# Optimization experiments

Hardware: AMD Instinct MI355X
Metric: run time of the kernel (lower is better)

Reference implementation:

```python
import jax, jax.numpy as jnp
import numpy as np

D_MODEL = 1024
NUM_HEADS = 16
HEAD_DIM = D_MODEL // NUM_HEADS


def setup_inputs() -> dict:
    key = jax.random.key(0)
    ks = jax.random.split(key, 10)
    B, SQ, SKV = 2, 2048, 2048
    s = 1.0 / np.sqrt(D_MODEL)
    inp = {
        "query": jax.random.normal(ks[0], (B, SQ, D_MODEL), jnp.float32),
        "key_value": jax.random.normal(ks[1], (B, SKV, D_MODEL), jnp.float32),
        "Wq": jax.random.normal(ks[2], (D_MODEL, D_MODEL), jnp.float32) * s,
        "bq": jnp.zeros((D_MODEL,), jnp.float32),
        "Wk": jax.random.normal(ks[3], (D_MODEL, D_MODEL), jnp.float32) * s,
        "bk": jnp.zeros((D_MODEL,), jnp.float32),
        "Wv": jax.random.normal(ks[4], (D_MODEL, D_MODEL), jnp.float32) * s,
        "bv": jnp.zeros((D_MODEL,), jnp.float32),
        "Wo": jax.random.normal(ks[5], (D_MODEL, D_MODEL), jnp.float32) * s,
        "bo": jnp.zeros((D_MODEL,), jnp.float32),
    }
    return inp


def reference(query, key_value, Wq, bq, Wk, bk, Wv, bv, Wo, bo):
    B, SQ, _ = query.shape
    SKV = key_value.shape[1]
    # projections (torch Linear: x @ W^T + b)
    Q = query @ Wq.T + bq
    K = key_value @ Wk.T + bk
    V = key_value @ Wv.T + bv
    # [B, H, S, Dh]
    Q = Q.reshape(B, SQ, NUM_HEADS, HEAD_DIM).transpose(0, 2, 1, 3)
    K = K.reshape(B, SKV, NUM_HEADS, HEAD_DIM).transpose(0, 2, 1, 3)
    V = V.reshape(B, SKV, NUM_HEADS, HEAD_DIM).transpose(0, 2, 1, 3)
    scores = jnp.einsum("bhqd,bhkd->bhqk", Q, K) / np.sqrt(HEAD_DIM)
    # causal mask: position q may attend to kv positions <= q
    causal = jnp.tril(jnp.ones((SQ, SKV), bool))  # True = keep
    scores = jnp.where(causal[None, None], scores, -jnp.inf)
    attn = jax.nn.softmax(scores, axis=-1)
    # dropout is identity in eval mode
    out = jnp.einsum("bhqk,bhkd->bhqd", attn, V)
    out = out.transpose(0, 2, 1, 3).reshape(B, SQ, D_MODEL)
    return out @ Wo.T + bo
```

## Files before the change

### kernel.cpp

```cpp
#include <hip/hip_runtime.h>
#include <hip/hip_bf16.h>
#include <cstdint>
#include <type_traits>

#define DM 1024
#define HEADS 16
#define DH 64
#define SEQ 2048
#define BATCH 2

typedef __attribute__((ext_vector_type(8))) short bf16x8;
typedef __attribute__((ext_vector_type(4))) float f32x4;
typedef __attribute__((ext_vector_type(16))) float f32x16;
typedef __attribute__((ext_vector_type(2))) unsigned int u32x2;
typedef __attribute__((ext_vector_type(4))) unsigned int u32x4;

#define SCALE2 0.18033688011112042f

#define GLOAD(dst, ptr) \
    asm volatile("global_load_dwordx4 %0, %1, off" : "=v"(dst) : "v"(ptr) : "memory")

static __device__ __forceinline__ unsigned short f2bf(float f) {
    unsigned u = __builtin_bit_cast(unsigned, f);
    u = u + 0x7fffu + ((u >> 16) & 1u);
    return (unsigned short)(u >> 16);
}

__global__ __launch_bounds__(256) void cast_all_k(
    const float* __restrict__ q, const float* __restrict__ kv,
    const float* __restrict__ wq, const float* __restrict__ wk,
    const float* __restrict__ wv, const float* __restrict__ wo,
    unsigned short* __restrict__ qb, unsigned short* __restrict__ kvb,
    unsigned short* __restrict__ wqb, unsigned short* __restrict__ wkb,
    unsigned short* __restrict__ wvb, unsigned short* __restrict__ wob)
{
    int blk = blockIdx.x;
    const float* s; unsigned short* d; int base;
    if (blk < 2048)      { s = q;  d = qb;  base = 0; }
    else if (blk < 4096) { s = kv; d = kvb; base = 2048; }
    else if (blk < 4608) { s = wq; d = wqb; base = 4096; }
    else if (blk < 5120) { s = wk; d = wkb; base = 4608; }
    else if (blk < 5632) { s = wv; d = wvb; base = 5120; }
    else                 { s = wo; d = wob; base = 5632; }
    int i = ((blk - base) * 256 + threadIdx.x) * 8;
    float4 a = *(const float4*)(s + i);
    float4 b2 = *(const float4*)(s + i + 4);
    ushort4 o0, o1;
    o0.x = f2bf(a.x);  o0.y = f2bf(a.y);  o0.z = f2bf(a.z);  o0.w = f2bf(a.w);
    o1.x = f2bf(b2.x); o1.y = f2bf(b2.y); o1.z = f2bf(b2.z); o1.w = f2bf(b2.w);
    *(ushort4*)(d + i) = o0;
    *(ushort4*)(d + i + 4) = o1;
}

template<int EPI>
__global__ __launch_bounds__(256) void gemm_nt(
    const unsigned short* __restrict__ A,
    const unsigned short* __restrict__ Bw,
    const float* __restrict__ biasA,
    const float* __restrict__ biasB,
    void* __restrict__ out0,
    void* __restrict__ out1,
    int M, int N, int K)
{
    constexpr int BK = 64;
    __shared__ alignas(16) unsigned short As[64 * BK];
    __shared__ alignas(16) unsigned short Bs[128 * BK];

    const int t = threadIdx.x;
    const int lane = t & 63;
    const int w = t >> 6;
    const int wn = w * 32;
    const int lr = lane & 15, lg = lane >> 4;
    const int m0 = blockIdx.x * 64, n0 = blockIdx.y * 128;

    f32x4 acc[4][2] = {};

    const int srow = t >> 3;
    const int schunk = t & 7;

    for (int kt = 0; kt < K; kt += BK) {
#pragma unroll
        for (int c = 0; c < 2; c++) {
            int row = srow + c * 32;
            int gc = schunk ^ (row & 7);
            __builtin_amdgcn_global_load_lds(
                (const __attribute__((address_space(1))) unsigned int*)(A + (size_t)(m0 + row) * K + kt + gc * 8),
                (__attribute__((address_space(3))) unsigned int*)(&As[row * BK + schunk * 8]), 16, 0, 0);
        }
#pragma unroll
        for (int c = 0; c < 4; c++) {
            int row = srow + c * 32;
            int gc = schunk ^ (row & 7);
            __builtin_amdgcn_global_load_lds(
                (const __attribute__((address_space(1))) unsigned int*)(Bw + (size_t)(n0 + row) * K + kt + gc * 8),
                (__attribute__((address_space(3))) unsigned int*)(&Bs[row * BK + schunk * 8]), 16, 0, 0);
        }
        __syncthreads();
#pragma unroll
        for (int kk = 0; kk < 2; kk++) {
            bf16x8 af[4], bfr[2];
#pragma unroll
            for (int i = 0; i < 4; i++)
                af[i] = *(const bf16x8*)(&As[(i * 16 + lr) * BK + (((kk * 4 + lg) ^ (lr & 7))) * 8]);
#pragma unroll
            for (int jj = 0; jj < 2; jj++)
                bfr[jj] = *(const bf16x8*)(&Bs[(wn + jj * 16 + lr) * BK + (((kk * 4 + lg) ^ (lr & 7))) * 8]);
#pragma unroll
            for (int i = 0; i < 4; i++)
#pragma unroll
                for (int jj = 0; jj < 2; jj++)
                    acc[i][jj] = __builtin_amdgcn_mfma_f32_16x16x32_bf16(af[i], bfr[jj], acc[i][jj], 0, 0, 0);
        }
        __syncthreads();
    }

    if constexpr (EPI == 0) {
        unsigned short* C = (unsigned short*)out0;
#pragma unroll
        for (int i = 0; i < 4; i++) {
            int rbase = m0 + i * 16 + lg * 4;
#pragma unroll
            for (int jj = 0; jj < 2; jj++) {
                int col = n0 + wn + jj * 16 + lr;
                float bv = biasA[col];
#pragma unroll
                for (int r = 0; r < 4; r++)
                    C[(size_t)(rbase + r) * 1024 + col] = f2bf((acc[i][jj][r] + bv) * SCALE2);
            }
        }
    } else if constexpr (EPI == 1) {
        if (n0 < 1024) {
            unsigned short* C = (unsigned short*)out0;
#pragma unroll
            for (int i = 0; i < 4; i++) {
                int rbase = m0 + i * 16 + lg * 4;
#pragma unroll
                for (int jj = 0; jj < 2; jj++) {
                    int col = n0 + wn + jj * 16 + lr;
                    float bv = biasA[col];
#pragma unroll
                    for (int r = 0; r < 4; r++)
                        C[(size_t)(rbase + r) * 1024 + col] = f2bf(acc[i][jj][r] + bv);
                }
            }
        } else {
            unsigned short* C = (unsigned short*)out1;
            int bidx = m0 >> 11;
#pragma unroll
            for (int i = 0; i < 4; i++) {
                int s0 = (m0 & 2047) + i * 16 + lg * 4;
#pragma unroll
                for (int jj = 0; jj < 2; jj++) {
                    int nv = n0 - 1024 + wn + jj * 16 + lr;
                    float bv = biasB[nv];
                    int hh = nv >> 6, dd = nv & 63;
                    ushort4 st;
                    st.x = f2bf(acc[i][jj][0] + bv);
                    st.y = f2bf(acc[i][jj][1] + bv);
                    st.z = f2bf(acc[i][jj][2] + bv);
                    st.w = f2bf(acc[i][jj][3] + bv);
                    *(ushort4*)(C + ((size_t)((bidx * HEADS + hh) * DH + dd)) * SEQ + s0) = st;
                }
            }
        }
    } else {
        float* C = (float*)out0;
#pragma unroll
        for (int i = 0; i < 4; i++) {
            int rbase = m0 + i * 16 + lg * 4;
#pragma unroll
            for (int jj = 0; jj < 2; jj++) {
                int col = n0 + wn + jj * 16 + lr;
                float bv = biasA[col];
#pragma unroll
                for (int r = 0; r < 4; r++)
                    C[(size_t)(rbase + r) * 1024 + col] = acc[i][jj][r] + bv;
            }
        }
    }
}

__global__ __launch_bounds__(256, 2) void attn_k(
    const unsigned short* __restrict__ Qp,
    const unsigned short* __restrict__ Kp,
    const unsigned short* __restrict__ Vt,
    unsigned short* __restrict__ Ctx)
{
    __shared__ alignas(16) unsigned char ldsb[2 * 16384];

    const int lane = threadIdx.x & 63;
    const int w = threadIdx.x >> 6;
    const int x = blockIdx.x;
    const int bh = x & 31;
    const int i16 = x >> 5;
    const int c = (i16 < 8) ? (2 * i16) : (31 - 2 * i16);
    const int b = bh >> 4, h = bh & 15;
    const int q0 = c * 128;
    const int lq = lane & 31;
    const int hi = lane >> 5;
    const int qq = q0 + w * 32 + lq;
    const int nb = 2 * c + 2;
    const int my_nb = (q0 + 32 * w + 95) >> 6;
    constexpr float THR = 11.5f;

    bf16x8 Qf[4];
    {
        u32x4 qtmp[4];
        const unsigned short* qb = Qp + (size_t)(b * SEQ + qq) * DM + h * DH + hi * 8;
#pragma unroll
        for (int d = 0; d < 4; d++) GLOAD(qtmp[d], qb + d * 16);
        asm volatile("s_waitcnt vmcnt(0)" ::: "memory");
        __builtin_amdgcn_sched_barrier(0);
#pragma unroll
        for (int d = 0; d < 4; d++) Qf[d] = __builtin_bit_cast(bf16x8, qtmp[d]);
    }

    const int colx = (((lane & 7) ^ (lane >> 3)) << 4);
    const char* kg[2];
    const char* vg[2];
#pragma unroll
    for (int u = 0; u < 2; u++) {
        int s = 2 * w + u;
        int row = 8 * s + (lane >> 3);
        kg[u] = (const char*)Kp + (((size_t)(b * SEQ + row) * DM + h * DH) * 2) + colx;
        vg[u] = (const char*)Vt + ((((size_t)(b * HEADS + h) * DH + row) * SEQ) * 2) + colx;
    }
    const int kxor = (lq & 7) << 4;

    auto stage = [&](int buf, int t) {
        int kboff_k = t * (64 * DM * 2);
        int kboff_v = t * 128;
#pragma unroll
        for (int u = 0; u < 2; u++) {
            int s = 2 * w + u;
            __builtin_amdgcn_global_load_lds(
                (const __attribute__((address_space(1))) unsigned int*)(kg[u] + kboff_k),
                (__attribute__((address_space(3))) unsigned int*)(&ldsb[buf * 16384 + s * 1024 + lane * 16]), 16, 0, 0);
            __builtin_amdgcn_global_load_lds(
                (const __attribute__((address_space(1))) unsigned int*)(vg[u] + kboff_v),
                (__attribute__((address_space(3))) unsigned int*)(&ldsb[buf * 16384 + 8192 + s * 1024 + lane * 16]), 16, 0, 0);
        }
    };

    f32x16 o0 = {}, o1 = {};
    float m_run = -1e30f, l_run = 0.f;
    const int qmh0 = qq - 4 * hi;

    stage(0, 0);

    for (int t = 0; t < nb; t++) {
        const int cur = t & 1;
        if (t + 1 < nb) {
            stage(cur ^ 1, t + 1);
            asm volatile("s_waitcnt vmcnt(4)" ::: "memory");
        } else {
            asm volatile("s_waitcnt vmcnt(0)" ::: "memory");
        }
        __builtin_amdgcn_sched_barrier(0);
        __builtin_amdgcn_s_barrier();

        if (t < my_nb) {
            const unsigned char* Kb = &ldsb[cur * 16384];
            const unsigned char* Vb = Kb + 8192;
            const int kb = t * 64;

            bf16x8 KA[4], KB[4], Vc[4][2];
#pragma unroll
            for (int d = 0; d < 4; d++) {
                int col = (d * 32 + hi * 16) ^ kxor;
                KA[d] = *(const bf16x8*)(Kb + lq * 128 + col);
                KB[d] = *(const bf16x8*)(Kb + (lq + 32) * 128 + col);
            }
#pragma unroll
            for (int s = 0; s < 4; s++)
#pragma unroll
                for (int dt = 0; dt < 2; dt++)
                    Vc[s][dt] = *(const bf16x8*)(Vb + (dt * 32 + lq) * 128 + ((s * 32 + hi * 16) ^ kxor));

            f32x16 sa0 = {}, sa1 = {};
            __builtin_amdgcn_s_setprio(1);
#pragma unroll
            for (int d = 0; d < 4; d++) {
                sa0 = __builtin_amdgcn_mfma_f32_32x32x16_bf16(KA[d], Qf[d], sa0, 0, 0, 0);
                sa1 = __builtin_amdgcn_mfma_f32_32x32x16_bf16(KB[d], Qf[d], sa1, 0, 0, 0);
            }
            __builtin_amdgcn_s_setprio(0);

            const int qmh = qmh0 - kb;
#pragma unroll
            for (int r = 0; r < 16; r++) {
                int kvl = (r & 3) + 8 * (r >> 2);
                sa0[r] = (kvl <= qmh) ? sa0[r] : -1e30f;
                sa1[r] = (kvl + 32 <= qmh) ? sa1[r] : -1e30f;
            }
            float mx[16];
#pragma unroll
            for (int r = 0; r < 16; r++) mx[r] = fmaxf(sa0[r], sa1[r]);
#pragma unroll
            for (int r = 0; r < 8; r++) mx[r] = fmaxf(mx[r], mx[r + 8]);
#pragma unroll
            for (int r = 0; r < 4; r++) mx[r] = fmaxf(mx[r], mx[r + 4]);
            mx[0] = fmaxf(mx[0], mx[2]);
            mx[1] = fmaxf(mx[1], mx[3]);
            float mloc = fmaxf(mx[0], mx[1]);
            mloc = fmaxf(mloc, __shfl_xor(mloc, 32));

            if (!__all(mloc - m_run <= THR)) {
                float m_new = fmaxf(m_run, mloc);
                float sf = __builtin_amdgcn_exp2f(m_run - m_new);
                l_run *= sf;
#pragma unroll
                for (int r = 0; r < 16; r++) { o0[r] *= sf; o1[r] *= sf; }
                m_run = m_new;
            }

            float p0v[16], p1v[16];
#pragma unroll
            for (int r = 0; r < 16; r++) {
                p0v[r] = __builtin_amdgcn_exp2f(sa0[r] - m_run);
                p1v[r] = __builtin_amdgcn_exp2f(sa1[r] - m_run);
            }
            float s4[8];
#pragma unroll
            for (int r = 0; r < 8; r++) s4[r] = (p0v[r] + p0v[r + 8]) + (p1v[r] + p1v[r + 8]);
#pragma unroll
            for (int r = 0; r < 4; r++) s4[r] += s4[r + 4];
            float ps = (s4[0] + s4[1]) + (s4[2] + s4[3]);
            ps += __shfl_xor(ps, 32);
            l_run += ps;

            unsigned c0[8], c1[8];
#pragma unroll
            for (int ii = 0; ii < 8; ii++) {
                unsigned pk;
                asm("v_cvt_pk_bf16_f32 %0, %1, %2" : "=v"(pk) : "v"(p0v[2 * ii]), "v"(p0v[2 * ii + 1]));
                c0[ii] = pk;
                asm("v_cvt_pk_bf16_f32 %0, %1, %2" : "=v"(pk) : "v"(p1v[2 * ii]), "v"(p1v[2 * ii + 1]));
                c1[ii] = pk;
            }
            bf16x8 Pb[4];
            {
                u32x2 r02 = __builtin_amdgcn_permlane32_swap(c0[0], c0[2], false, false);
                u32x2 r13 = __builtin_amdgcn_permlane32_swap(c0[1], c0[3], false, false);
                u32x2 r46 = __builtin_amdgcn_permlane32_swap(c0[4], c0[6], false, false);
                u32x2 r57 = __builtin_amdgcn_permlane32_swap(c0[5], c0[7], false, false);
                u32x4 w0 = {r02.x, r13.x, r02.y, r13.y};
                u32x4 w1 = {r46.x, r57.x, r46.y, r57.y};
                Pb[0] = __builtin_bit_cast(bf16x8, w0);
                Pb[1] = __builtin_bit_cast(bf16x8, w1);
            }
            {
                u32x2 r02 = __builtin_amdgcn_permlane32_swap(c1[0], c1[2], false, false);
                u32x2 r13 = __builtin_amdgcn_permlane32_swap(c1[1], c1[3], false, false);
                u32x2 r46 = __builtin_amdgcn_permlane32_swap(c1[4], c1[6], false, false);
                u32x2 r57 = __builtin_amdgcn_permlane32_swap(c1[5], c1[7], false, false);
                u32x4 w0 = {r02.x, r13.x, r02.y, r13.y};
                u32x4 w1 = {r46.x, r57.x, r46.y, r57.y};
                Pb[2] = __builtin_bit_cast(bf16x8, w0);
                Pb[3] = __builtin_bit_cast(bf16x8, w1);
            }

            __builtin_amdgcn_s_setprio(1);
#pragma unroll
            for (int s = 0; s < 4; s++) {
                o0 = __builtin_amdgcn_mfma_f32_32x32x16_bf16(Vc[s][0], Pb[s], o0, 0, 0, 0);
                o1 = __builtin_amdgcn_mfma_f32_32x32x16_bf16(Vc[s][1], Pb[s], o1, 0, 0, 0);
            }
            __builtin_amdgcn_s_setprio(0);
        }
        __builtin_amdgcn_s_barrier();
    }

    float inv = 1.0f / l_run;
    unsigned short* cb = Ctx + (size_t)(b * SEQ + qq) * DM + h * DH + hi * 4;
#pragma unroll
    for (int g = 0; g < 4; g++) {
        ushort4 s0, s1;
        s0.x = f2bf(o0[4 * g + 0] * inv); s0.y = f2bf(o0[4 * g + 1] * inv);
        s0.z = f2bf(o0[4 * g + 2] * inv); s0.w = f2bf(o0[4 * g + 3] * inv);
        s1.x = f2bf(o1[4 * g + 0] * inv); s1.y = f2bf(o1[4 * g + 1] * inv);
        s1.z = f2bf(o1[4 * g + 2] * inv); s1.w = f2bf(o1[4 * g + 3] * inv);
        *(ushort4*)(cb + g * 8) = s0;
        *(ushort4*)(cb + 32 + g * 8) = s1;
    }
}

extern "C" void kernel_launch(void* const* d_in, const int* in_sizes, int n_in,
                              void* d_out, int out_size, void* d_ws, size_t ws_size,
                              hipStream_t stream)
{
    const float* query = (const float*)d_in[0];
    const float* keyv  = (const float*)d_in[1];
    const float* Wq = (const float*)d_in[2];
    const float* bq = (const float*)d_in[3];
    const float* Wk = (const float*)d_in[4];
    const float* bk = (const float*)d_in[5];
    const float* Wv = (const float*)d_in[6];
    const float* bv = (const float*)d_in[7];
    const float* Wo = (const float*)d_in[8];
    const float* bo = (const float*)d_in[9];
    float* out = (float*)d_out;

    const int M = BATCH * SEQ;
    char* ws = (char*)d_ws;
    size_t off = 0;
    auto alloc = [&](size_t elems) { unsigned short* p = (unsigned short*)(ws + off); off += elems * 2; return p; };
    unsigned short* qb  = alloc((size_t)M * DM);
    unsigned short* kvb = alloc((size_t)M * DM);
    unsigned short* wqb = alloc((size_t)DM * DM);
    unsigned short* wkb = alloc((size_t)DM * DM);
    unsigned short* wvb = alloc((size_t)DM * DM);
    unsigned short* wob = alloc((size_t)DM * DM);
    unsigned short* Qp  = alloc((size_t)M * DM);
    unsigned short* Kp  = alloc((size_t)M * DM);
    unsigned short* Vt  = alloc((size_t)M * DM);
    unsigned short* Ctx = alloc((size_t)M * DM);

    cast_all_k<<<6144, 256, 0, stream>>>(query, keyv, Wq, Wk, Wv, Wo,
                                         qb, kvb, wqb, wkb, wvb, wob);

    gemm_nt<0><<<dim3(M / 64, 8),  256, 0, stream>>>(qb,  wqb, bq, nullptr, Qp, nullptr, M, DM, DM);
    gemm_nt<1><<<dim3(M / 64, 16), 256, 0, stream>>>(kvb, wkb, bk, bv,      Kp, Vt,      M, 2 * DM, DM);

    attn_k<<<dim3(512), 256, 0, stream>>>(Qp, Kp, Vt, Ctx);

    gemm_nt<2><<<dim3(M / 64, 8),  256, 0, stream>>>(Ctx, wob, bo, nullptr, out, nullptr, M, DM, DM);
}
```

Measured before the change: 119.8 us.

## Split causal attention KV range across blocks and add a combine kernel

Query chunks with longer causal KV ranges are split into 2–4 blocks, each covering a contiguous KV slice. The grid grows from 512 to 1280 blocks, which is meant to even out the per-block work imbalance that comes from the causal mask. Each split writes unnormalized bf16 partial outputs plus its running max and sum into workspace regions whose earlier contents are no longer needed. A new combine kernel merges the partials with log-sum-exp weights. The cost is an extra launch, extra global traffic for the partials, and an added bf16 rounding step on the partial outputs.

After: 122.3 us. 1.02x slower.

```diff
diff --git a/kernel.cpp b/kernel.cpp
--- a/kernel.cpp
+++ b/kernel.cpp
@@ -24,6 +24,9 @@
     unsigned u = __builtin_bit_cast(unsigned, f);
     u = u + 0x7fffu + ((u >> 16) & 1u);
     return (unsigned short)(u >> 16);
+}
+static __device__ __forceinline__ float bf2f(unsigned short us) {
+    return __builtin_bit_cast(float, (unsigned)us << 16);
 }
 
 __global__ __launch_bounds__(256) void cast_all_k(
@@ -184,7 +187,9 @@
     const unsigned short* __restrict__ Qp,
     const unsigned short* __restrict__ Kp,
     const unsigned short* __restrict__ Vt,
-    unsigned short* __restrict__ Ctx)
+    unsigned short* __restrict__ Ctx,
+    unsigned short* __restrict__ pO,
+    float2* __restrict__ pML)
 {
     __shared__ alignas(16) unsigned char ldsb[2 * 16384];
 
@@ -192,14 +197,22 @@
     const int w = threadIdx.x >> 6;
     const int x = blockIdx.x;
     const int bh = x & 31;
-    const int i16 = x >> 5;
-    const int c = (i16 < 8) ? (2 * i16) : (31 - 2 * i16);
+    const int g = x >> 5;
+    int c, p, S;
+    if (g < 4)       { c = g;                    p = 0;            S = 1; }
+    else if (g < 12) { c = 4 + ((g - 4) >> 1);   p = (g - 4) & 1;  S = 2; }
+    else if (g < 24) { c = 8 + (g - 12) / 3;     p = (g - 12) % 3; S = 3; }
+    else             { c = 12 + ((g - 24) >> 2); p = (g - 24) & 3; S = 4; }
+    const int nb = 2 * c + 2;
+    const int len0 = (nb + S - 1) / S;
+    const int start = p * len0;
+    const int len = min(len0, nb - start);
+
     const int b = bh >> 4, h = bh & 15;
     const int q0 = c * 128;
     const int lq = lane & 31;
     const int hi = lane >> 5;
     const int qq = q0 + w * 32 + lq;
-    const int nb = 2 * c + 2;
     const int my_nb = (q0 + 32 * w + 95) >> 6;
     constexpr float THR = 11.5f;
 
@@ -246,11 +259,12 @@
     float m_run = -1e30f, l_run = 0.f;
     const int qmh0 = qq - 4 * hi;
 
-    stage(0, 0);
-
-    for (int t = 0; t < nb; t++) {
-        const int cur = t & 1;
-        if (t + 1 < nb) {
+    stage(0, start);
+
+    for (int it = 0; it < len; it++) {
+        const int t = start + it;
+        const int cur = it & 1;
+        if (it + 1 < len) {
             stage(cur ^ 1, t + 1);
             asm volatile("s_waitcnt vmcnt(4)" ::: "memory");
         } else {
@@ -371,17 +385,98 @@
         __builtin_amdgcn_s_barrier();
     }
 
-    float inv = 1.0f / l_run;
-    unsigned short* cb = Ctx + (size_t)(b * SEQ + qq) * DM + h * DH + hi * 4;
-#pragma unroll
-    for (int g = 0; g < 4; g++) {
+    if (S == 1) {
+        float inv = 1.0f / l_run;
+        unsigned short* cb = Ctx + (size_t)(b * SEQ + qq) * DM + h * DH + hi * 4;
+#pragma unroll
+        for (int gg = 0; gg < 4; gg++) {
+            ushort4 s0, s1;
+            s0.x = f2bf(o0[4 * gg + 0] * inv); s0.y = f2bf(o0[4 * gg + 1] * inv);
+            s0.z = f2bf(o0[4 * gg + 2] * inv); s0.w = f2bf(o0[4 * gg + 3] * inv);
+            s1.x = f2bf(o1[4 * gg + 0] * inv); s1.y = f2bf(o1[4 * gg + 1] * inv);
+            s1.z = f2bf(o1[4 * gg + 2] * inv); s1.w = f2bf(o1[4 * gg + 3] * inv);
+            *(ushort4*)(cb + gg * 8) = s0;
+            *(ushort4*)(cb + 32 + gg * 8) = s1;
+        }
+        return;
+    }
+
+    const int slot = g - 4;
+    const int qrow = w * 32 + lq;
+    unsigned short* pb = pO + ((size_t)(bh * 36 + slot) * 8192) + qrow * 64 + hi * 4;
+#pragma unroll
+    for (int gg = 0; gg < 4; gg++) {
         ushort4 s0, s1;
-        s0.x = f2bf(o0[4 * g + 0] * inv); s0.y = f2bf(o0[4 * g + 1] * inv);
-        s0.z = f2bf(o0[4 * g + 2] * inv); s0.w = f2bf(o0[4 * g + 3] * inv);
-        s1.x = f2bf(o1[4 * g + 0] * inv); s1.y = f2bf(o1[4 * g + 1] * inv);
-        s1.z = f2bf(o1[4 * g + 2] * inv); s1.w = f2bf(o1[4 * g + 3] * inv);
-        *(ushort4*)(cb + g * 8) = s0;
-        *(ushort4*)(cb + 32 + g * 8) = s1;
+        s0.x = f2bf(o0[4 * gg + 0]); s0.y = f2bf(o0[4 * gg + 1]);
+        s0.z = f2bf(o0[4 * gg + 2]); s0.w = f2bf(o0[4 * gg + 3]);
+        s1.x = f2bf(o1[4 * gg + 0]); s1.y = f2bf(o1[4 * gg + 1]);
+        s1.z = f2bf(o1[4 * gg + 2]); s1.w = f2bf(o1[4 * gg + 3]);
+        *(ushort4*)(pb + gg * 8) = s0;
+        *(ushort4*)(pb + 32 + gg * 8) = s1;
+    }
+    if (hi == 0)
+        pML[(size_t)(bh * 36 + slot) * 128 + qrow] = make_float2(m_run, l_run);
+}
+
+__global__ __launch_bounds__(256) void combine_k(
+    const unsigned short* __restrict__ pO,
+    const float2* __restrict__ pML,
+    unsigned short* __restrict__ Ctx)
+{
+    const int x = blockIdx.x;
+    const int bh = x & 31;
+    const int c = (x >> 5) + 4;
+    const int S = (c >> 2) + 1;
+    int slot0;
+    if (c < 8)       slot0 = 2 * (c - 4);
+    else if (c < 12) slot0 = 8 + 3 * (c - 8);
+    else             slot0 = 20 + 4 * (c - 12);
+    const int b = bh >> 4, h = bh & 15;
+
+    const int q = threadIdx.x >> 1;
+    const int d0 = (threadIdx.x & 1) * 32;
+
+    float m[4], l[4], wgt[4];
+    float M = -1e30f;
+#pragma unroll
+    for (int i = 0; i < 4; i++) {
+        if (i < S) {
+            float2 ml = pML[(size_t)(bh * 36 + slot0 + i) * 128 + q];
+            m[i] = ml.x; l[i] = ml.y;
+            M = fmaxf(M, m[i]);
+        }
+    }
+    float L = 0.f;
+#pragma unroll
+    for (int i = 0; i < 4; i++) {
+        if (i < S) {
+            wgt[i] = __builtin_amdgcn_exp2f(m[i] - M);
+            L += l[i] * wgt[i];
+        }
+    }
+    float invL = 1.0f / L;
+#pragma unroll
+    for (int i = 0; i < 4; i++) if (i < S) wgt[i] *= invL;
+
+    unsigned short* cb = Ctx + (size_t)(b * SEQ + c * 128 + q) * DM + h * DH + d0;
+#pragma unroll
+    for (int dd = 0; dd < 32; dd += 8) {
+        float acc[8] = {};
+#pragma unroll
+        for (int i = 0; i < 4; i++) {
+            if (i < S) {
+                const unsigned short* pp = pO + ((size_t)(bh * 36 + slot0 + i) * 8192) + q * 64 + d0 + dd;
+                bf16x8 v = *(const bf16x8*)pp;
+#pragma unroll
+                for (int e = 0; e < 8; e++)
+                    acc[e] += wgt[i] * bf2f((unsigned short)v[e]);
+            }
+        }
+        ushort4 s0, s1;
+        s0.x = f2bf(acc[0]); s0.y = f2bf(acc[1]); s0.z = f2bf(acc[2]); s0.w = f2bf(acc[3]);
+        s1.x = f2bf(acc[4]); s1.y = f2bf(acc[5]); s1.z = f2bf(acc[6]); s1.w = f2bf(acc[7]);
+        *(ushort4*)(cb + dd) = s0;
+        *(ushort4*)(cb + dd + 4) = s1;
     }
 }
 
@@ -416,13 +511,17 @@
     unsigned short* Vt  = alloc((size_t)M * DM);
     unsigned short* Ctx = alloc((size_t)M * DM);
 
+    unsigned short* pO  = (unsigned short*)(ws + 0);
+    float2*         pML = (float2*)(ws + 20971520);
+
     cast_all_k<<<6144, 256, 0, stream>>>(query, keyv, Wq, Wk, Wv, Wo,
                                          qb, kvb, wqb, wkb, wvb, wob);
 
     gemm_nt<0><<<dim3(M / 64, 8),  256, 0, stream>>>(qb,  wqb, bq, nullptr, Qp, nullptr, M, DM, DM);
     gemm_nt<1><<<dim3(M / 64, 16), 256, 0, stream>>>(kvb, wkb, bk, bv,      Kp, Vt,      M, 2 * DM, DM);
 
-    attn_k<<<dim3(512), 256, 0, stream>>>(Qp, Kp, Vt, Ctx);
+    attn_k<<<dim3(1280), 256, 0, stream>>>(Qp, Kp, Vt, Ctx, pO, pML);
+    combine_k<<<dim3(384), 256, 0, stream>>>(pO, pML, Ctx);
 
     gemm_nt<2><<<dim3(M / 64, 8),  256, 0, stream>>>(Ctx, wob, bo, nullptr, out, nullptr, M, DM, DM);
 }
```
